# Kernel optimization log

Measured on AMD Instinct MI355X. Metric: run time of the kernel, lower is better.

Reference implementation:

```python
import jax, jax.numpy as jnp
import numpy as np

E = 256   # embed_dim
L = 64    # num_landmarks
C = 256   # in_channels
N_ITER = 6


def iterative_inv(K):
    # Newton-Schulz pseudo-inverse on small [*, L, L] matrices (faithful to torch code)
    I = jnp.eye(K.shape[-1], dtype=K.dtype)
    KA = jnp.abs(K)
    V0 = KA.sum(axis=-2, keepdims=True).max(axis=-1, keepdims=True)  # [*,1,1]
    VI = KA.sum(axis=-1, keepdims=True).max(axis=-2, keepdims=True)  # [*,1,1]
    V = jnp.swapaxes(K, -1, -2) / (V0 * VI)
    for _ in range(N_ITER):
        KV = K @ V
        V = 0.25 * V @ (13.0 * I - KV @ (15.0 * I - KV @ (7.0 * I - KV)))
    return V


def setup_inputs() -> dict:
    key = jax.random.key(0)
    k0, k1, k2 = jax.random.split(key, 3)
    x = jax.random.normal(k0, (8, C, 64, 64), dtype=jnp.float32)
    # Conv2d 1x1 weights stored as [out, in]
    w_qkv = jax.random.normal(k1, (3 * E, C), dtype=jnp.float32) * 0.02
    b_qkv = jnp.zeros((3 * E,), dtype=jnp.float32)
    w_out = jax.random.normal(k2, (C, E), dtype=jnp.float32) * 0.02
    b_out = jnp.zeros((C,), dtype=jnp.float32)
    return {"x": x, "w_qkv": w_qkv, "b_qkv": b_qkv, "w_out": w_out, "b_out": b_out}


def reference(x, w_qkv, b_qkv, w_out, b_out):
    N, Cin, H, W = x.shape
    HW = H * W
    # 1x1 conv: [N, 3E, H, W]
    y = jnp.einsum('nchw,ec->nehw', x, w_qkv) + b_qkv[None, :, None, None]
    # faithful raw reshape (mixes channel/spatial like the torch code)
    qkv = y.reshape(N, HW, 3 * E)
    q, k, v = jnp.split(qkv, 3, axis=-1)                     # each [N, HW, E]
    scale = HW ** 0.5
    q_land = q.reshape(N, L, HW // L, E).mean(axis=-2) / scale  # [N, L, E]
    k_land = k.reshape(N, L, HW // L, E).mean(axis=-2) / scale  # [N, L, E]
    # three softmaxes, all over dim=-2 as in the original
    k1 = jax.nn.softmax(jnp.einsum('nie,nje->nij', q, k_land), axis=-2)       # [N, HW, L]
    k2 = jax.nn.softmax(jnp.einsum('nie,nje->nij', q_land, k_land), axis=-2)  # [N, L, L]
    k3 = jax.nn.softmax(jnp.einsum('nie,nje->nij', q_land, k), axis=-2)       # [N, L, HW]
    k2_inv = iterative_inv(k2)
    out = k1 @ (k2_inv @ (k3 @ v)) + v                        # [N, HW, E]
    out = out.reshape(N, E, H, W)                             # faithful raw reshape
    return jnp.einsum('nehw,ce->nchw', out, w_out) + b_out[None, :, None, None]
```

## Files before the change

### kernel.cpp

```cpp
#include <hip/hip_runtime.h>
#include <hip/hip_bf16.h>

typedef unsigned short u16;
typedef __attribute__((ext_vector_type(4))) float f32x4;
typedef __attribute__((ext_vector_type(8))) short short8;

#define NB   8
#define CIN  256
#define EDIM 256
#define M3   768
#define HWN  4096
#define LND  64
#define NS2  72

__device__ __forceinline__ float bf2f(u16 u){ return __uint_as_float(((unsigned)u)<<16); }
__device__ __forceinline__ u16 f2bf(float f){ __hip_bfloat16 h = __float2bfloat16(f); return *reinterpret_cast<u16*>(&h); }
__device__ __forceinline__ void bf2x2(unsigned u, float &lo, float &hi){
  lo = __uint_as_float(u<<16);
  hi = __uint_as_float(u & 0xffff0000u);
}

typedef __attribute__((address_space(1))) unsigned as1_uint;
typedef __attribute__((address_space(3))) unsigned as3_uint;
__device__ __forceinline__ void gl16(const void* g, void* l){
  __builtin_amdgcn_global_load_lds((const as1_uint*)g, (as3_uint*)l, 16, 0, 0);
}

__global__ __launch_bounds__(256) void k_prep(const float* __restrict__ x, u16* __restrict__ Xt,
                                              const float* __restrict__ wq, const float* __restrict__ wo,
                                              u16* __restrict__ Wqb, u16* __restrict__ Wob){
  const int bi = blockIdx.x;
  const int tid = threadIdx.x;
  if(bi >= 2048){
    int ti = (bi-2048)*256 + tid;
    const float* src; u16* dst;
    if(ti < 1536){ src = wq + (size_t)ti*128;        dst = Wqb + (size_t)ti*128; }
    else         { src = wo + (size_t)(ti-1536)*128; dst = Wob + (size_t)(ti-1536)*128; }
    #pragma unroll
    for(int t=0;t<128;t+=8){
      float4 v0 = *(const float4*)(src+t);
      float4 v1 = *(const float4*)(src+t+4);
      ushort4 o0, o1;
      o0.x=f2bf(v0.x); o0.y=f2bf(v0.y); o0.z=f2bf(v0.z); o0.w=f2bf(v0.w);
      o1.x=f2bf(v1.x); o1.y=f2bf(v1.y); o1.z=f2bf(v1.z); o1.w=f2bf(v1.w);
      *(ushort4*)(dst+t)   = o0;
      *(ushort4*)(dst+t+4) = o1;
    }
    return;
  }
  __shared__ float Ts[64*65];
  const int n = bi>>8, rem = bi&255, ct = rem>>6, pt = rem&63;
  const int c0 = ct*64, p0 = pt*64;
  {
    int cc = tid>>2, pj = (tid&3)*16;
    const float* xp = x + (size_t)n*CIN*HWN + (size_t)(c0+cc)*HWN + p0 + pj;
    #pragma unroll
    for(int j=0;j<16;j++) Ts[cc*65 + pj + j] = xp[j];
  }
  __syncthreads();
  {
    int pp = tid>>2, ej = (tid&3)*16;
    u16* op = Xt + ((size_t)n*HWN + p0 + pp)*CIN + c0 + ej;
    ushort4 o[4];
    #pragma unroll
    for(int j=0;j<16;j++) ((u16*)o)[j] = f2bf(Ts[(ej+j)*65 + pp]);
    *(ushort4*)(op+0)  = o[0];
    *(ushort4*)(op+4)  = o[1];
    *(ushort4*)(op+8)  = o[2];
    *(ushort4*)(op+12) = o[3];
  }
}

__global__ __launch_bounds__(256) void k_qkv(const u16* __restrict__ Wb, const u16* __restrict__ Xt,
                                             const float* __restrict__ bias, u16* __restrict__ Y){
  __shared__ __align__(16) u16 As[128*64];
  __shared__ __align__(16) u16 Bs[128*64];
  const int bi = blockIdx.x;
  const int n = bi&7, rem = bi>>3;
  const int ch0 = (rem%6)*128, p0 = (rem/6)*128;
  const int tid = threadIdx.x, lane = tid&63;
  const int c = tid&15, qq = (tid>>4)&3, w4 = tid>>6;
  const int wr0 = (w4&1)*64, wc0 = (w4>>1)*64;
  const u16* xb = Xt + ((size_t)n*HWN + p0)*CIN;
  const u16* wb = Wb + (size_t)ch0*CIN;
  f32x4 acc[4][4];
  #pragma unroll
  for(int mt=0;mt<4;mt++)
    #pragma unroll
    for(int nt=0;nt<4;nt++){ acc[mt][nt][0]=0.f; acc[mt][nt][1]=0.f; acc[mt][nt][2]=0.f; acc[mt][nt][3]=0.f; }
  const int srow  = w4*8 + (lane>>3);
  const int dslot = lane&7;
  const int sgo   = (dslot ^ (lane>>3))*8;
  const int rdswz = (c&7);
  for(int ph=0; ph<4; ph++){
    #pragma unroll
    for(int j=0;j<4;j++){
      int r = j*32 + srow;
      gl16(wb + (size_t)r*CIN + ph*64 + sgo, &As[r*64 + dslot*8]);
    }
    #pragma unroll
    for(int j=0;j<4;j++){
      int r = j*32 + srow;
      gl16(xb + (size_t)r*CIN + ph*64 + sgo, &Bs[r*64 + dslot*8]);
    }
    __syncthreads();
    #pragma unroll
    for(int kt=0;kt<2;kt++){
      short8 af[4], bff[4];
      const int rslot = ((kt*4+qq)^rdswz)*8;
      #pragma unroll
      for(int mt=0;mt<4;mt++) af[mt]  = *(const short8*)&As[(wr0+mt*16+c)*64 + rslot];
      #pragma unroll
      for(int nt=0;nt<4;nt++) bff[nt] = *(const short8*)&Bs[(wc0+nt*16+c)*64 + rslot];
      #pragma unroll
      for(int mt=0;mt<4;mt++)
        #pragma unroll
        for(int nt=0;nt<4;nt++)
          acc[mt][nt] = __builtin_amdgcn_mfma_f32_16x16x32_bf16(af[mt], bff[nt], acc[mt][nt], 0, 0, 0);
    }
    __syncthreads();
  }
  u16* Yb = Y + (size_t)n*M3*HWN;
  #pragma unroll
  for(int mt=0;mt<4;mt++){
    int chb = ch0 + wr0 + mt*16 + 4*qq;
    float b0 = bias[chb], b1 = bias[chb+1], b2 = bias[chb+2], b3 = bias[chb+3];
    #pragma unroll
    for(int nt=0;nt<4;nt++){
      int p = p0 + wc0 + nt*16 + c;
      u16* yp = Yb + (size_t)chb*HWN + p;
      yp[0]             = f2bf(acc[mt][nt][0]+b0);
      yp[HWN]           = f2bf(acc[mt][nt][1]+b1);
      yp[2*(size_t)HWN] = f2bf(acc[mt][nt][2]+b2);
      yp[3*(size_t)HWN] = f2bf(acc[mt][nt][3]+b3);
    }
  }
}

__global__ void k_land(const u16* __restrict__ Y, float* __restrict__ qland, float* __restrict__ kland){
  const int l = blockIdx.x, n = blockIdx.y, e = threadIdx.x;
  const u16* base = Y + (size_t)n*M3*HWN;
  float qs=0.f, ks=0.f;
  #pragma unroll 8
  for(int m=0;m<64;m++){
    size_t off = (size_t)(l*64+m)*M3;
    qs += bf2f(base[off+e]);
    ks += bf2f(base[off+256+e]);
  }
  qland[((size_t)n*LND+l)*EDIM+e] = qs*(1.f/4096.f);
  kland[((size_t)n*LND+l)*EDIM+e] = ks*(1.f/4096.f);
}

__device__ __forceinline__ void ns_mm2(const u16* L, int sL, const u16* Rt, int sR,
                                       int wv, int q, int c, f32x4 r4[4]){
  short8 a0 = *(const short8*)(L + (size_t)(16*wv + c)*sL + 8*q);
  short8 a1 = *(const short8*)(L + (size_t)(16*wv + c)*sL + 32 + 8*q);
  #pragma unroll
  for(int tc=0;tc<4;tc++){
    f32x4 acc = {0.f,0.f,0.f,0.f};
    short8 b0 = *(const short8*)(Rt + (size_t)(16*tc + c)*sR + 8*q);
    short8 b1 = *(const short8*)(Rt + (size_t)(16*tc + c)*sR + 32 + 8*q);
    acc = __builtin_amdgcn_mfma_f32_16x16x32_bf16(a0, b0, acc, 0, 0, 0);
    acc = __builtin_amdgcn_mfma_f32_16x16x32_bf16(a1, b1, acc, 0, 0, 0);
    r4[tc] = acc;
  }
}

#define TTS 64
__device__ void ns_body(int n, char* smem, const float* __restrict__ qland,
                        const float* __restrict__ kland, float* __restrict__ KinvT){
  u16* Kb  = (u16*)(smem + 0);
  u16* Vb  = (u16*)(smem + 9216);
  u16* Vt  = (u16*)(smem + 18432);
  u16* KVb = (u16*)(smem + 27648);
  u16* KVt = (u16*)(smem + 36864);
  u16* Tt  = (u16*)(smem + 46080);
  float* sS   = (float*)(smem + 27648);
  float* sred = (float*)(smem + 44544);
  const int tid = threadIdx.x;
  const int wv = tid>>6, q = (tid>>4)&3, c = tid&15;
  const float* qb = qland + (size_t)n*LND*EDIM;
  const float* kb = kland + (size_t)n*LND*EDIM;
  f32x4 acc[4];
  #pragma unroll
  for(int t=0;t<4;t++){ acc[t][0]=0.f; acc[t][1]=0.f; acc[t][2]=0.f; acc[t][3]=0.f; }
  for(int e0=0;e0<EDIM;e0+=64){
    __syncthreads();
    {
      int row = tid>>2, c0 = (tid&3)*16;
      const float* qp = qb + (size_t)row*EDIM + e0 + c0;
      const float* kp = kb + (size_t)row*EDIM + e0 + c0;
      u16* qd = &KVb[row*NS2 + c0];
      u16* kd = &KVt[row*NS2 + c0];
      #pragma unroll
      for(int j=0;j<16;j+=4){
        float4 qv = *(const float4*)(qp+j);
        float4 kv = *(const float4*)(kp+j);
        ushort4 qo, ko;
        qo.x=f2bf(qv.x); qo.y=f2bf(qv.y); qo.z=f2bf(qv.z); qo.w=f2bf(qv.w);
        ko.x=f2bf(kv.x); ko.y=f2bf(kv.y); ko.z=f2bf(kv.z); ko.w=f2bf(kv.w);
        *(ushort4*)(qd+j) = qo;
        *(ushort4*)(kd+j) = ko;
      }
    }
    __syncthreads();
    {
      short8 a0 = *(const short8*)&KVb[(16*wv+c)*NS2 + 8*q];
      short8 a1 = *(const short8*)&KVb[(16*wv+c)*NS2 + 32 + 8*q];
      #pragma unroll
      for(int tc=0;tc<4;tc++){
        short8 b0 = *(const short8*)&KVt[(16*tc+c)*NS2 + 8*q];
        short8 b1 = *(const short8*)&KVt[(16*tc+c)*NS2 + 32 + 8*q];
        acc[tc] = __builtin_amdgcn_mfma_f32_16x16x32_bf16(a0, b0, acc[tc], 0, 0, 0);
        acc[tc] = __builtin_amdgcn_mfma_f32_16x16x32_bf16(a1, b1, acc[tc], 0, 0, 0);
      }
    }
  }
  __syncthreads();
  #pragma unroll
  for(int tc=0;tc<4;tc++){
    int col = 16*tc + c, row0 = 16*wv + 4*q;
    sS[(row0+0)*66+col] = acc[tc][0];
    sS[(row0+1)*66+col] = acc[tc][1];
    sS[(row0+2)*66+col] = acc[tc][2];
    sS[(row0+3)*66+col] = acc[tc][3];
  }
  __syncthreads();
  if(tid < 64){
    int j = tid;
    float m = -1e30f;
    for(int i=0;i<64;i++) m = fmaxf(m, sS[i*66+j]);
    float ssum = 0.f;
    for(int i=0;i<64;i++) ssum += __expf(sS[i*66+j]-m);
    float inv = 1.f/ssum, cs = 0.f;
    for(int i=0;i<64;i++){
      float kv = __expf(sS[i*66+j]-m)*inv;
      cs += fabsf(kv);
      Kb[i*NS2+j] = f2bf(kv);
    }
    sred[j] = cs;
  }
  __syncthreads();
  if(tid < 64){
    int i = tid; float rs = 0.f;
    for(int j=0;j<64;j++) rs += fabsf(bf2f(Kb[i*NS2+j]));
    sred[64+i] = rs;
  }
  __syncthreads();
  if(tid == 0){
    float v0=-1e30f, vi=-1e30f;
    for(int t=0;t<64;t++){ v0 = fmaxf(v0, sred[t]); vi = fmaxf(vi, sred[64+t]); }
    sred[128] = 1.f/(v0*vi);
  }
  __syncthreads();
  {
    float sc = sred[128];
    int i = tid>>2, j16 = (tid&3)*16;
    #pragma unroll
    for(int jj=0;jj<16;jj++){
      int j = j16+jj;
      u16 bvv = f2bf(bf2f(Kb[j*NS2+i])*sc);
      Vb[i*NS2+j] = bvv;
      Vt[j*NS2+i] = bvv;
    }
  }
  __syncthreads();
  f32x4 r4[4];
  for(int it=0; it<6; it++){
    ns_mm2(Kb, NS2, Vt, NS2, wv, q, c, r4);
    #pragma unroll
    for(int tc=0;tc<4;tc++){
      int col = 16*tc + c, row0 = 16*wv + 4*q;
      ushort4 pk;
      pk.x = f2bf(r4[tc][0]); pk.y = f2bf(r4[tc][1]); pk.z = f2bf(r4[tc][2]); pk.w = f2bf(r4[tc][3]);
      KVb[(row0+0)*NS2+col] = pk.x; KVb[(row0+1)*NS2+col] = pk.y;
      KVb[(row0+2)*NS2+col] = pk.z; KVb[(row0+3)*NS2+col] = pk.w;
      *(ushort4*)&KVt[(size_t)col*NS2 + row0] = pk;
    }
    __syncthreads();
    ns_mm2(KVb, NS2, KVt, NS2, wv, q, c, r4);
    #pragma unroll
    for(int tc=0;tc<4;tc++){
      int col = 16*tc+c, row0 = 16*wv+4*q;
      ushort4 pk;
      #pragma unroll
      for(int r=0;r<4;r++){
        float kvv = bf2f(KVb[(row0+r)*NS2+col]);
        ((u16*)&pk)[r] = f2bf(7.f*kvv - r4[tc][r]);
      }
      *(ushort4*)&Tt[(size_t)col*TTS + row0] = pk;
    }
    __syncthreads();
    ns_mm2(KVb, NS2, Tt, TTS, wv, q, c, r4);
    __syncthreads();
    #pragma unroll
    for(int tc=0;tc<4;tc++){
      int col = 16*tc+c, row0 = 16*wv+4*q;
      ushort4 pk;
      #pragma unroll
      for(int r=0;r<4;r++){
        float kvv = bf2f(KVb[(row0+r)*NS2+col]);
        ((u16*)&pk)[r] = f2bf(15.f*kvv - r4[tc][r]);
      }
      *(ushort4*)&Tt[(size_t)col*TTS + row0] = pk;
    }
    __syncthreads();
    ns_mm2(Vb, NS2, Tt, TTS, wv, q, c, r4);
    __syncthreads();
    #pragma unroll
    for(int tc=0;tc<4;tc++){
      int col = 16*tc+c, row0 = 16*wv+4*q;
      float nv[4]; ushort4 pk;
      #pragma unroll
      for(int r=0;r<4;r++){
        float vv = bf2f(Vb[(row0+r)*NS2+col]);
        nv[r] = 0.25f*(13.f*vv - r4[tc][r]);
        u16 bb = f2bf(nv[r]);
        Vb[(row0+r)*NS2+col] = bb;
        ((u16*)&pk)[r] = bb;
      }
      *(ushort4*)&Vt[(size_t)col*NS2 + row0] = pk;
      if(it==5){
        *(float4*)&KinvT[(size_t)n*4096 + (size_t)col*64 + row0] = make_float4(nv[0],nv[1],nv[2],nv[3]);
      }
    }
    __syncthreads();
  }
}

#define LGS 264
__global__ __launch_bounds__(256) void k_landgemm(const u16* __restrict__ Y, const float* __restrict__ qland,
                                                  const float* __restrict__ kland, float* __restrict__ Z1,
                                                  float* __restrict__ Z3, float* __restrict__ KinvT){
  __shared__ __align__(16) char usm[54272];
  const int z = blockIdx.y;
  if(blockIdx.x == 64){
    if((z&1)==0) ns_body(z>>1, usm, qland, kland, KinvT);
    return;
  }
  u16* As = (u16*)usm;
  u16* BsU = (u16*)(usm + 33792);
  const int n = z>>1, which = z&1;
  const int b0 = blockIdx.x*64;
  const float* land = (which ? qland : kland) + (size_t)n*LND*EDIM;
  const int boff = which ? 256 : 0;
  float* out = (which ? Z3 : Z1) + (size_t)n*LND*HWN;
  const u16* Yb = Y + (size_t)n*M3*HWN + boff;
  const int tid = threadIdx.x, lane = tid&63;
  const int c = tid&15, qq = (tid>>4)&3, wv = tid>>6;
  {
    int r = tid>>2, c0 = (tid&3)*64;
    const float* lp = land + (size_t)r*EDIM + c0;
    u16* dp = &As[r*LGS + c0];
    #pragma unroll
    for(int j=0;j<64;j+=4){
      float4 v = *(const float4*)(lp+j);
      ushort4 o; o.x=f2bf(v.x); o.y=f2bf(v.y); o.z=f2bf(v.z); o.w=f2bf(v.w);
      *(ushort4*)(dp+j) = o;
    }
  }
  const int srow  = wv*8 + (lane>>3);
  const int dslot = lane&7;
  const int sgo   = (dslot ^ (lane>>3))*8;
  const int rdswz = (c&7);
  f32x4 acc[4];
  #pragma unroll
  for(int nt=0;nt<4;nt++){ acc[nt][0]=0.f; acc[nt][1]=0.f; acc[nt][2]=0.f; acc[nt][3]=0.f; }
  #pragma unroll
  for(int j=0;j<2;j++){
    int r = j*32 + srow;
    gl16(Yb + (size_t)(b0+r)*M3 + sgo, BsU + r*64 + dslot*8);
  }
  __syncthreads();
  for(int ph=0; ph<4; ph++){
    const int cur = ph&1;
    if(ph<3){
      #pragma unroll
      for(int j=0;j<2;j++){
        int r = j*32 + srow;
        gl16(Yb + (size_t)(b0+r)*M3 + (ph+1)*64 + sgo, BsU + (cur^1)*4096 + r*64 + dslot*8);
      }
    }
    #pragma unroll
    for(int kt=0;kt<2;kt++){
      short8 af = *(const short8*)&As[(16*wv + c)*LGS + ph*64 + kt*32 + qq*8];
      const int rslot = ((kt*4+qq)^rdswz)*8;
      #pragma unroll
      for(int nt=0;nt<4;nt++){
        short8 bff = *(const short8*)&BsU[cur*4096 + (nt*16+c)*64 + rslot];
        acc[nt] = __builtin_amdgcn_mfma_f32_16x16x32_bf16(af, bff, acc[nt], 0, 0, 0);
      }
    }
    __syncthreads();
  }
  const int m0 = 16*wv + 4*qq;
  #pragma unroll
  for(int nt=0;nt<4;nt++){
    int col = b0 + nt*16 + c;
    out[(size_t)(m0+0)*HWN + col] = acc[nt][0];
    out[(size_t)(m0+1)*HWN + col] = acc[nt][1];
    out[(size_t)(m0+2)*HWN + col] = acc[nt][2];
    out[(size_t)(m0+3)*HWN + col] = acc[nt][3];
  }
}

__device__ void soft3_body(int idx, char* smem, const float* __restrict__ Z3, u16* __restrict__ P){
  const int kc = idx&31, n = idx>>5;
  const int tid = threadIdx.x, jb = kc*128;
  float* Sf   = (float*)smem;
  float* sinv = (float*)(smem + 33792);
  const float* z3b = Z3 + (size_t)n*LND*HWN;
  {
    int ibase = (tid>>5)*8, j4 = (tid&31)*4;
    #pragma unroll
    for(int r=0;r<8;r++){
      int i = ibase + r;
      *(float4*)&Sf[i*132 + j4] = *(const float4*)&z3b[(size_t)i*HWN + jb + j4];
    }
  }
  __syncthreads();
  if(tid < 128){
    int j = tid;
    float m = -1e30f;
    for(int i=0;i<64;i++) m = fmaxf(m, Sf[i*132 + j]);
    float s = 0.f;
    for(int i=0;i<64;i++){ float e = __expf(Sf[i*132 + j] - m); Sf[i*132 + j] = e; s += e; }
    sinv[j] = 1.f/s;
  }
  __syncthreads();
  {
    int i = tid>>2, j0 = (tid&3)*32;
    u16* pp = P + ((size_t)n*LND + i)*HWN + jb + j0;
    #pragma unroll
    for(int t=0;t<32;t+=4){
      ushort4 o;
      o.x = f2bf(Sf[i*132 + j0+t+0]*sinv[j0+t+0]);
      o.y = f2bf(Sf[i*132 + j0+t+1]*sinv[j0+t+1]);
      o.z = f2bf(Sf[i*132 + j0+t+2]*sinv[j0+t+2]);
      o.w = f2bf(Sf[i*132 + j0+t+3]*sinv[j0+t+3]);
      *(ushort4*)(pp+t) = o;
    }
  }
}

__device__ void soft1_body(int b, char* smem, float* __restrict__ Z1){
  const int n = b>>6, j = b&63, tid = threadIdx.x;
  float* redm = (float*)smem;
  float* reds = redm + 4;
  float* base = Z1 + ((size_t)n*LND + j)*HWN;
  float v[16];
  float m = -1e30f;
  #pragma unroll
  for(int r=0;r<16;r++){ v[r] = base[r*256 + tid]; m = fmaxf(m, v[r]); }
  #pragma unroll
  for(int o=32;o;o>>=1) m = fmaxf(m, __shfl_xor(m, o));
  const int wid = tid>>6;
  if((tid&63)==0) redm[wid] = m;
  __syncthreads();
  m = fmaxf(fmaxf(redm[0],redm[1]), fmaxf(redm[2],redm[3]));
  float s = 0.f;
  #pragma unroll
  for(int r=0;r<16;r++){ v[r] = __expf(v[r]-m); s += v[r]; }
  #pragma unroll
  for(int o=32;o;o>>=1) s += __shfl_xor(s, o);
  if((tid&63)==0) reds[wid] = s;
  __syncthreads();
  s = reds[0]+reds[1]+reds[2]+reds[3];
  float inv = 1.f/s;
  #pragma unroll
  for(int r=0;r<16;r++) base[r*256 + tid] = v[r]*inv;
}

__global__ __launch_bounds__(256) void k_mega(const float* __restrict__ Z3, u16* __restrict__ P,
                                              float* __restrict__ Z1){
  __shared__ __align__(16) char smem[34304];
  const int bi = blockIdx.x;
  if(bi < 256) soft3_body(bi, smem, Z3, P);
  else         soft1_body(bi-256, smem, Z1);
}

__global__ __launch_bounds__(256) void k_pv(const u16* __restrict__ P, const u16* __restrict__ Y,
                                            float* __restrict__ part){
  __shared__ __align__(16) u16 As[64*64];
  __shared__ __align__(16) u16 Vt[128*64];
  const int bi = blockIdx.x;
  const int kc = bi&31, n = (bi>>5)&7, eh = bi>>8;
  const int jb = kc*128, eb = eh*128;
  const int tid = threadIdx.x, lane = tid&63;
  const int c = tid&15, qq = (tid>>4)&3, wv = tid>>6;
  const u16* Pb = P + (size_t)n*LND*HWN;
  const u16* Yb = Y + (size_t)n*M3*HWN;
  const int srow  = wv*8 + (lane>>3);
  const int dslot = lane&7;
  const int sgo   = (dslot ^ (lane>>3))*8;
  const int rdswz = (c&7);
  f32x4 acc[4][2];
  #pragma unroll
  for(int mt=0;mt<4;mt++)
    #pragma unroll
    for(int nt=0;nt<2;nt++){ acc[mt][nt][0]=0.f; acc[mt][nt][1]=0.f; acc[mt][nt][2]=0.f; acc[mt][nt][3]=0.f; }
  for(int ph=0; ph<2; ph++){
    #pragma unroll
    for(int j=0;j<2;j++){
      int r = j*32 + srow;
      gl16(Pb + (size_t)r*HWN + jb + ph*64 + sgo, &As[r*64 + dslot*8]);
    }
    #pragma unroll
    for(int rep=0; rep<4; rep++){
      int jl = (tid>>4) + 16*rep;
      int ec = (tid&15)*8;
      uint4 U = *(const uint4*)&Yb[(size_t)(jb+ph*64+jl)*M3 + 512 + eb + ec];
      const u16* uv = (const u16*)&U;
      #pragma unroll
      for(int k=0;k<8;k++){
        int e = ec+k;
        int slot = ((jl>>3) ^ (e&7) ^ ((e>>3)&7)) & 7;
        Vt[e*64 + slot*8 + (jl&7)] = uv[k];
      }
    }
    __syncthreads();
    #pragma unroll
    for(int kt=0;kt<2;kt++){
      const int rslotA = ((kt*4+qq)^rdswz)*8;
      short8 af[4];
      #pragma unroll
      for(int mt=0;mt<4;mt++) af[mt] = *(const short8*)&As[(mt*16+c)*64 + rslotA];
      #pragma unroll
      for(int nt=0;nt<2;nt++){
        int e = wv*32 + nt*16 + c;
        int slotB = ((kt*4+qq) ^ (e&7) ^ ((e>>3)&7)) & 7;
        short8 bf_ = *(const short8*)&Vt[e*64 + slotB*8];
        #pragma unroll
        for(int mt=0;mt<4;mt++)
          acc[mt][nt] = __builtin_amdgcn_mfma_f32_16x16x32_bf16(af[mt], bf_, acc[mt][nt], 0, 0, 0);
      }
    }
    __syncthreads();
  }
  float* pb = part + ((size_t)n*32 + kc)*LND*EDIM + eb;
  #pragma unroll
  for(int mt=0;mt<4;mt++){
    int row0 = mt*16 + 4*qq;
    #pragma unroll
    for(int nt=0;nt<2;nt++){
      int e = wv*32 + nt*16 + c;
      pb[(size_t)(row0+0)*EDIM + e] = acc[mt][nt][0];
      pb[(size_t)(row0+1)*EDIM + e] = acc[mt][nt][1];
      pb[(size_t)(row0+2)*EDIM + e] = acc[mt][nt][2];
      pb[(size_t)(row0+3)*EDIM + e] = acc[mt][nt][3];
    }
  }
}

__global__ void k_fred(const float* __restrict__ part, float* __restrict__ B3){
  const int idx = blockIdx.x*256 + threadIdx.x;
  const int n = idx >> 14, rem = idx & 16383;
  const float* p = part + (size_t)n*32*16384 + rem;
  float s = 0.f;
  #pragma unroll
  for(int kc=0;kc<32;kc++) s += p[(size_t)kc*16384];
  B3[idx] = s;
}

__global__ __launch_bounds__(256) void k_c2(const float* __restrict__ KinvT, const float* __restrict__ B3,
                                            float* __restrict__ C2){
  const int eb = blockIdx.x*64, n = blockIdx.y, tid = threadIdx.x;
  __shared__ float KT[64][68];
  __shared__ float Bs2[64][68];
  {
    int l = tid>>2, o16 = (tid&3)*16;
    const float* kp = KinvT + (size_t)n*4096 + l*64 + o16;
    const float* bp = B3 + ((size_t)n*LND + l)*EDIM + eb + o16;
    #pragma unroll
    for(int t=0;t<16;t+=4){
      *(float4*)&KT[l][o16+t]  = *(const float4*)(kp+t);
      *(float4*)&Bs2[l][o16+t] = *(const float4*)(bp+t);
    }
  }
  __syncthreads();
  const int j0 = (tid>>4)*4, u0 = (tid&15)*4;
  float acc[4][4] = {};
  #pragma unroll 8
  for(int l=0;l<64;l++){
    f32x4 a = *(f32x4*)&KT[l][j0];
    f32x4 b = *(f32x4*)&Bs2[l][u0];
    #pragma unroll
    for(int s=0;s<4;s++)
      #pragma unroll
      for(int u=0;u<4;u++) acc[s][u] += a[s]*b[u];
  }
  #pragma unroll
  for(int s=0;s<4;s++){
    float4 fv = make_float4(acc[s][0],acc[s][1],acc[s][2],acc[s][3]);
    *(float4*)&C2[((size_t)n*LND + j0+s)*EDIM + eb + u0] = fv;
  }
}

__global__ __launch_bounds__(256) void k_out(const float* __restrict__ Z1, const float* __restrict__ C2,
                                             const u16* __restrict__ Y, u16* __restrict__ OM){
  const int ib = blockIdx.x*64, n = blockIdx.y, tid = threadIdx.x;
  __shared__ float K1s[64][68];
  __shared__ u16 C2s[64*264];
  {
    int j = tid>>2, i16 = (tid&3)*16;
    const float* zp = Z1 + ((size_t)n*LND + j)*HWN + ib + i16;
    #pragma unroll
    for(int t=0;t<16;t+=4) *(float4*)&K1s[j][i16+t] = *(const float4*)(zp+t);
    int e64 = (tid&3)*64;
    const float* cp = C2 + ((size_t)n*LND + j)*EDIM + e64;
    #pragma unroll
    for(int t=0;t<64;t+=4){
      float4 v = *(const float4*)(cp+t);
      C2s[j*264 + e64+t+0] = f2bf(v.x);
      C2s[j*264 + e64+t+1] = f2bf(v.y);
      C2s[j*264 + e64+t+2] = f2bf(v.z);
      C2s[j*264 + e64+t+3] = f2bf(v.w);
    }
  }
  __syncthreads();
  const int i0 = (tid>>4)*4, e0 = (tid&15)*16;
  float acc[4][16] = {};
  for(int j=0;j<64;j++){
    f32x4 a = *(f32x4*)&K1s[j][i0];
    const u16* cb = &C2s[j*264 + e0];
    uint4 U0 = *(const uint4*)cb;
    uint4 U1 = *(const uint4*)(cb+8);
    float bv[16];
    bf2x2(U0.x, bv[0], bv[1]);  bf2x2(U0.y, bv[2], bv[3]);
    bf2x2(U0.z, bv[4], bv[5]);  bf2x2(U0.w, bv[6], bv[7]);
    bf2x2(U1.x, bv[8], bv[9]);  bf2x2(U1.y, bv[10], bv[11]);
    bf2x2(U1.z, bv[12], bv[13]); bf2x2(U1.w, bv[14], bv[15]);
    #pragma unroll
    for(int u=0;u<16;u++){
      acc[0][u] += a[0]*bv[u];
      acc[1][u] += a[1]*bv[u];
      acc[2][u] += a[2]*bv[u];
      acc[3][u] += a[3]*bv[u];
    }
  }
  const u16* Yb = Y + (size_t)n*M3*HWN;
  u16* ob = OM + (size_t)n*HWN*EDIM;
  #pragma unroll
  for(int s=0;s<4;s++){
    int i = ib + i0 + s;
    const u16* vp = Yb + (size_t)i*M3 + 512 + e0;
    uint4 U0 = *(const uint4*)vp, U1 = *(const uint4*)(vp+8);
    float vv[16];
    bf2x2(U0.x, vv[0], vv[1]);  bf2x2(U0.y, vv[2], vv[3]);
    bf2x2(U0.z, vv[4], vv[5]);  bf2x2(U0.w, vv[6], vv[7]);
    bf2x2(U1.x, vv[8], vv[9]);  bf2x2(U1.y, vv[10], vv[11]);
    bf2x2(U1.z, vv[12], vv[13]); bf2x2(U1.w, vv[14], vv[15]);
    #pragma unroll
    for(int t=0;t<16;t+=4){
      ushort4 o;
      o.x = f2bf(acc[s][t+0]+vv[t+0]);
      o.y = f2bf(acc[s][t+1]+vv[t+1]);
      o.z = f2bf(acc[s][t+2]+vv[t+2]);
      o.w = f2bf(acc[s][t+3]+vv[t+3]);
      *(ushort4*)&ob[(size_t)i*EDIM + e0 + t] = o;
    }
  }
}

__global__ __launch_bounds__(256) void k_trans2(const u16* __restrict__ OM, u16* __restrict__ OMT){
  __shared__ u16 Ts[64*65];
  const int bi = blockIdx.x;
  const int n = bi>>8, rem = bi&255, et = rem>>6, pt = rem&63;
  const int e0 = et*64, p0 = pt*64, tid = threadIdx.x;
  const u16* omb = OM + (size_t)n*HWN*EDIM;
  {
    int ee = tid>>2, pj = (tid&3)*16;
    const u16* ip = omb + (size_t)(e0+ee)*HWN + p0 + pj;
    ushort4 v0 = *(const ushort4*)(ip);
    ushort4 v1 = *(const ushort4*)(ip+4);
    ushort4 v2 = *(const ushort4*)(ip+8);
    ushort4 v3 = *(const ushort4*)(ip+12);
    u16* tp = &Ts[ee*65 + pj];
    tp[0]=v0.x; tp[1]=v0.y; tp[2]=v0.z; tp[3]=v0.w;
    tp[4]=v1.x; tp[5]=v1.y; tp[6]=v1.z; tp[7]=v1.w;
    tp[8]=v2.x; tp[9]=v2.y; tp[10]=v2.z; tp[11]=v2.w;
    tp[12]=v3.x; tp[13]=v3.y; tp[14]=v3.z; tp[15]=v3.w;
  }
  __syncthreads();
  {
    int pp = tid>>2, ej = (tid&3)*16;
    u16* op = OMT + ((size_t)n*HWN + p0 + pp)*EDIM + e0 + ej;
    ushort4 o[4];
    #pragma unroll
    for(int j=0;j<16;j++) ((u16*)o)[j] = Ts[(ej+j)*65 + pp];
    *(ushort4*)(op+0)  = o[0];
    *(ushort4*)(op+4)  = o[1];
    *(ushort4*)(op+8)  = o[2];
    *(ushort4*)(op+12) = o[3];
  }
}

__global__ __launch_bounds__(256) void k_proj(const u16* __restrict__ Wb, const u16* __restrict__ OMT,
                                              const float* __restrict__ bias, float* __restrict__ out){
  __shared__ __align__(16) u16 As[128*64];
  __shared__ __align__(16) u16 Bs[128*64];
  const int bi = blockIdx.x;
  const int n = bi&7, rem = bi>>3;
  const int ch0 = (rem&1)*128, p0 = (rem>>1)*128;
  const int tid = threadIdx.x, lane = tid&63;
  const int c = tid&15, qq = (tid>>4)&3, w4 = tid>>6;
  const int wr0 = (w4&1)*64, wc0 = (w4>>1)*64;
  const u16* xb = OMT + ((size_t)n*HWN + p0)*EDIM;
  const u16* wb = Wb + (size_t)ch0*EDIM;
  f32x4 acc[4][4];
  #pragma unroll
  for(int mt=0;mt<4;mt++)
    #pragma unroll
    for(int nt=0;nt<4;nt++){ acc[mt][nt][0]=0.f; acc[mt][nt][1]=0.f; acc[mt][nt][2]=0.f; acc[mt][nt][3]=0.f; }
  const int srow  = w4*8 + (lane>>3);
  const int dslot = lane&7;
  const int sgo   = (dslot ^ (lane>>3))*8;
  const int rdswz = (c&7);
  for(int ph=0; ph<4; ph++){
    #pragma unroll
    for(int j=0;j<4;j++){
      int r = j*32 + srow;
      gl16(wb + (size_t)r*EDIM + ph*64 + sgo, &As[r*64 + dslot*8]);
    }
    #pragma unroll
    for(int j=0;j<4;j++){
      int r = j*32 + srow;
      gl16(xb + (size_t)r*EDIM + ph*64 + sgo, &Bs[r*64 + dslot*8]);
    }
    __syncthreads();
    #pragma unroll
    for(int kt=0;kt<2;kt++){
      short8 af[4], bff[4];
      const int rslot = ((kt*4+qq)^rdswz)*8;
      #pragma unroll
      for(int mt=0;mt<4;mt++) af[mt]  = *(const short8*)&As[(wr0+mt*16+c)*64 + rslot];
      #pragma unroll
      for(int nt=0;nt<4;nt++) bff[nt] = *(const short8*)&Bs[(wc0+nt*16+c)*64 + rslot];
      #pragma unroll
      for(int mt=0;mt<4;mt++)
        #pragma unroll
        for(int nt=0;nt<4;nt++)
          acc[mt][nt] = __builtin_amdgcn_mfma_f32_16x16x32_bf16(af[mt], bff[nt], acc[mt][nt], 0, 0, 0);
    }
    __syncthreads();
  }
  float* ob = out + (size_t)n*EDIM*HWN;
  #pragma unroll
  for(int mt=0;mt<4;mt++){
    int chb = ch0 + wr0 + mt*16 + 4*qq;
    float b0 = bias[chb], b1 = bias[chb+1], b2 = bias[chb+2], b3 = bias[chb+3];
    #pragma unroll
    for(int nt=0;nt<4;nt++){
      int p = p0 + wc0 + nt*16 + c;
      float* yp = ob + (size_t)chb*HWN + p;
      yp[0]             = acc[mt][nt][0]+b0;
      yp[HWN]           = acc[mt][nt][1]+b1;
      yp[2*(size_t)HWN] = acc[mt][nt][2]+b2;
      yp[3*(size_t)HWN] = acc[mt][nt][3]+b3;
    }
  }
}

extern "C" void kernel_launch(void* const* d_in, const int* in_sizes, int n_in,
                              void* d_out, int out_size, void* d_ws, size_t ws_size,
                              hipStream_t stream){
  (void)out_size; (void)ws_size;
  const float* x     = (const float*)d_in[0];
  const float* w_qkv = (const float*)d_in[1];
  const float* b_qkv = (const float*)d_in[2];
  const float* w_out = (const float*)d_in[3];
  const float* b_out = (const float*)d_in[4];
  for(int i=0;i<n_in;i++){
    switch(in_sizes[i]){
      case 8388608: x     = (const float*)d_in[i]; break;
      case 196608:  w_qkv = (const float*)d_in[i]; break;
      case 768:     b_qkv = (const float*)d_in[i]; break;
      case 65536:   w_out = (const float*)d_in[i]; break;
      case 256:     b_out = (const float*)d_in[i]; break;
      default: break;
    }
  }
  float* out = (float*)d_out;
  char* ws = (char*)d_ws;

  u16*   Y     = (u16*)(ws + 0);
  float* qland = (float*)(ws + 50331648);
  float* kland = (float*)(ws + 50855936);
  float* Z1    = (float*)(ws + 51380224);
  float* Z3    = (float*)(ws + 59768832);
  float* KinvT = (float*)(ws + 68157440);
  u16*   Xt    = (u16*)(ws + 68288512);
  float* part  = (float*)(ws + 68288512);
  u16*   OMT   = (u16*)(ws + 68288512);
  float* B3    = (float*)(ws + 85065728);
  float* C2    = (float*)(ws + 85590016);
  u16*   OM    = (u16*)(ws + 86114304);
  u16*   Pbuf  = (u16*)(ws + 86114304);
  u16*   Wqb   = (u16*)(ws + 59768832);
  u16*   Wob   = (u16*)(ws + 102891520);

  k_prep    <<<dim3(2056),   256, 0, stream>>>(x, Xt, w_qkv, w_out, Wqb, Wob);
  k_qkv     <<<dim3(1536),   256, 0, stream>>>(Wqb, Xt, b_qkv, Y);
  k_land    <<<dim3(64,8),   256, 0, stream>>>(Y, qland, kland);
  k_landgemm<<<dim3(65,16),  256, 0, stream>>>(Y, qland, kland, Z1, Z3, KinvT);
  k_mega    <<<dim3(768),    256, 0, stream>>>(Z3, Pbuf, Z1);
  k_pv      <<<dim3(512),    256, 0, stream>>>(Pbuf, Y, part);
  k_fred    <<<dim3(512),    256, 0, stream>>>(part, B3);
  k_c2      <<<dim3(4,8),    256, 0, stream>>>(KinvT, B3, C2);
  k_out     <<<dim3(64,8),   256, 0, stream>>>(Z1, C2, Y, OM);
  k_trans2  <<<dim3(2048),   256, 0, stream>>>(OM, OMT);
  k_proj    <<<dim3(512),    256, 0, stream>>>(Wob, OMT, b_out, out);
}
```

Before: 220.8 us.

## Fuse split-K reduction into k_c2, use MFMA in k_out, drop transpose kernel

New measurement: 211.5 us. -4.2%, faster.

```diff
diff --git a/kernel.cpp b/kernel.cpp
--- a/kernel.cpp
+++ b/kernel.cpp
@@ -552,30 +552,34 @@
   }
 }
 
-__global__ void k_fred(const float* __restrict__ part, float* __restrict__ B3){
-  const int idx = blockIdx.x*256 + threadIdx.x;
-  const int n = idx >> 14, rem = idx & 16383;
-  const float* p = part + (size_t)n*32*16384 + rem;
-  float s = 0.f;
-  #pragma unroll
-  for(int kc=0;kc<32;kc++) s += p[(size_t)kc*16384];
-  B3[idx] = s;
-}
-
-__global__ __launch_bounds__(256) void k_c2(const float* __restrict__ KinvT, const float* __restrict__ B3,
-                                            float* __restrict__ C2){
+__global__ __launch_bounds__(256) void k_c2(const float* __restrict__ KinvT, const float* __restrict__ part,
+                                            u16* __restrict__ C2T){
   const int eb = blockIdx.x*64, n = blockIdx.y, tid = threadIdx.x;
   __shared__ float KT[64][68];
   __shared__ float Bs2[64][68];
+  __shared__ u16 Ct[64*72];
   {
     int l = tid>>2, o16 = (tid&3)*16;
     const float* kp = KinvT + (size_t)n*4096 + l*64 + o16;
-    const float* bp = B3 + ((size_t)n*LND + l)*EDIM + eb + o16;
-    #pragma unroll
-    for(int t=0;t<16;t+=4){
-      *(float4*)&KT[l][o16+t]  = *(const float4*)(kp+t);
-      *(float4*)&Bs2[l][o16+t] = *(const float4*)(bp+t);
-    }
+    #pragma unroll
+    for(int t=0;t<16;t+=4) *(float4*)&KT[l][o16+t] = *(const float4*)(kp+t);
+    const float* pp = part + (size_t)n*32*16384 + (size_t)l*256 + eb + o16;
+    float4 s0 = {0,0,0,0}, s1 = {0,0,0,0}, s2 = {0,0,0,0}, s3 = {0,0,0,0};
+    for(int kc=0;kc<32;kc++){
+      const float* b = pp + (size_t)kc*16384;
+      float4 v0 = *(const float4*)(b);
+      float4 v1 = *(const float4*)(b+4);
+      float4 v2 = *(const float4*)(b+8);
+      float4 v3 = *(const float4*)(b+12);
+      s0.x+=v0.x; s0.y+=v0.y; s0.z+=v0.z; s0.w+=v0.w;
+      s1.x+=v1.x; s1.y+=v1.y; s1.z+=v1.z; s1.w+=v1.w;
+      s2.x+=v2.x; s2.y+=v2.y; s2.z+=v2.z; s2.w+=v2.w;
+      s3.x+=v3.x; s3.y+=v3.y; s3.z+=v3.z; s3.w+=v3.w;
+    }
+    *(float4*)&Bs2[l][o16+0]  = s0;
+    *(float4*)&Bs2[l][o16+4]  = s1;
+    *(float4*)&Bs2[l][o16+8]  = s2;
+    *(float4*)&Bs2[l][o16+12] = s3;
   }
   __syncthreads();
   const int j0 = (tid>>4)*4, u0 = (tid&15)*4;
@@ -590,122 +594,99 @@
       for(int u=0;u<4;u++) acc[s][u] += a[s]*b[u];
   }
   #pragma unroll
-  for(int s=0;s<4;s++){
-    float4 fv = make_float4(acc[s][0],acc[s][1],acc[s][2],acc[s][3]);
-    *(float4*)&C2[((size_t)n*LND + j0+s)*EDIM + eb + u0] = fv;
-  }
-}
-
-__global__ __launch_bounds__(256) void k_out(const float* __restrict__ Z1, const float* __restrict__ C2,
+  for(int s=0;s<4;s++)
+    #pragma unroll
+    for(int u=0;u<4;u++)
+      Ct[(u0+u)*72 + j0+s] = f2bf(acc[s][u]);
+  __syncthreads();
+  {
+    int e = tid>>2, j16 = (tid&3)*16;
+    u16* op = C2T + ((size_t)n*256 + eb + e)*64 + j16;
+    #pragma unroll
+    for(int t=0;t<16;t+=4)
+      *(ushort4*)(op+t) = *(const ushort4*)&Ct[e*72 + j16 + t];
+  }
+}
+
+__global__ __launch_bounds__(256) void k_out(const float* __restrict__ Z1, const u16* __restrict__ C2T,
                                              const u16* __restrict__ Y, u16* __restrict__ OM){
-  const int ib = blockIdx.x*64, n = blockIdx.y, tid = threadIdx.x;
-  __shared__ float K1s[64][68];
-  __shared__ u16 C2s[64*264];
+  __shared__ __align__(16) u16 Cs[256*64];
+  __shared__ __align__(16) u16 Zt[64*72];
+  const int ib = blockIdx.x*64, n = blockIdx.y;
+  const int tid = threadIdx.x, lane = tid&63;
+  const int c = tid&15, qq = (tid>>4)&3, wv = tid>>6;
+  const int srow  = wv*8 + (lane>>3);
+  const int dslot = lane&7;
+  const int sgo   = (dslot ^ (lane>>3))*8;
+  const int rdswz = (c&7);
+  const u16* cb = C2T + (size_t)n*256*64;
+  #pragma unroll
+  for(int j=0;j<8;j++){
+    int r = j*32 + srow;
+    gl16(cb + (size_t)r*64 + sgo, &Cs[r*64 + dslot*8]);
+  }
   {
     int j = tid>>2, i16 = (tid&3)*16;
     const float* zp = Z1 + ((size_t)n*LND + j)*HWN + ib + i16;
     #pragma unroll
-    for(int t=0;t<16;t+=4) *(float4*)&K1s[j][i16+t] = *(const float4*)(zp+t);
-    int e64 = (tid&3)*64;
-    const float* cp = C2 + ((size_t)n*LND + j)*EDIM + e64;
-    #pragma unroll
-    for(int t=0;t<64;t+=4){
-      float4 v = *(const float4*)(cp+t);
-      C2s[j*264 + e64+t+0] = f2bf(v.x);
-      C2s[j*264 + e64+t+1] = f2bf(v.y);
-      C2s[j*264 + e64+t+2] = f2bf(v.z);
-      C2s[j*264 + e64+t+3] = f2bf(v.w);
-    }
-  }
-  __syncthreads();
-  const int i0 = (tid>>4)*4, e0 = (tid&15)*16;
-  float acc[4][16] = {};
-  for(int j=0;j<64;j++){
-    f32x4 a = *(f32x4*)&K1s[j][i0];
-    const u16* cb = &C2s[j*264 + e0];
-    uint4 U0 = *(const uint4*)cb;
-    uint4 U1 = *(const uint4*)(cb+8);
-    float bv[16];
-    bf2x2(U0.x, bv[0], bv[1]);  bf2x2(U0.y, bv[2], bv[3]);
-    bf2x2(U0.z, bv[4], bv[5]);  bf2x2(U0.w, bv[6], bv[7]);
-    bf2x2(U1.x, bv[8], bv[9]);  bf2x2(U1.y, bv[10], bv[11]);
-    bf2x2(U1.z, bv[12], bv[13]); bf2x2(U1.w, bv[14], bv[15]);
-    #pragma unroll
-    for(int u=0;u<16;u++){
-      acc[0][u] += a[0]*bv[u];
-      acc[1][u] += a[1]*bv[u];
-      acc[2][u] += a[2]*bv[u];
-      acc[3][u] += a[3]*bv[u];
-    }
+    for(int t=0;t<16;t+=4){
+      float4 v = *(const float4*)(zp+t);
+      Zt[(i16+t+0)*72 + j] = f2bf(v.x);
+      Zt[(i16+t+1)*72 + j] = f2bf(v.y);
+      Zt[(i16+t+2)*72 + j] = f2bf(v.z);
+      Zt[(i16+t+3)*72 + j] = f2bf(v.w);
+    }
+  }
+  __syncthreads();
+  f32x4 acc[4][4];
+  #pragma unroll
+  for(int mt=0;mt<4;mt++)
+    #pragma unroll
+    for(int nt=0;nt<4;nt++){ acc[mt][nt][0]=0.f; acc[mt][nt][1]=0.f; acc[mt][nt][2]=0.f; acc[mt][nt][3]=0.f; }
+  #pragma unroll
+  for(int kt=0;kt<2;kt++){
+    const int rslot = ((kt*4+qq)^rdswz)*8;
+    short8 af[4], bf_[4];
+    #pragma unroll
+    for(int mt=0;mt<4;mt++) af[mt] = *(const short8*)&Cs[(wv*64+mt*16+c)*64 + rslot];
+    #pragma unroll
+    for(int nt=0;nt<4;nt++) bf_[nt] = *(const short8*)&Zt[(nt*16+c)*72 + kt*32 + qq*8];
+    #pragma unroll
+    for(int mt=0;mt<4;mt++)
+      #pragma unroll
+      for(int nt=0;nt<4;nt++)
+        acc[mt][nt] = __builtin_amdgcn_mfma_f32_16x16x32_bf16(af[mt], bf_[nt], acc[mt][nt], 0, 0, 0);
   }
   const u16* Yb = Y + (size_t)n*M3*HWN;
   u16* ob = OM + (size_t)n*HWN*EDIM;
   #pragma unroll
-  for(int s=0;s<4;s++){
-    int i = ib + i0 + s;
-    const u16* vp = Yb + (size_t)i*M3 + 512 + e0;
-    uint4 U0 = *(const uint4*)vp, U1 = *(const uint4*)(vp+8);
-    float vv[16];
-    bf2x2(U0.x, vv[0], vv[1]);  bf2x2(U0.y, vv[2], vv[3]);
-    bf2x2(U0.z, vv[4], vv[5]);  bf2x2(U0.w, vv[6], vv[7]);
-    bf2x2(U1.x, vv[8], vv[9]);  bf2x2(U1.y, vv[10], vv[11]);
-    bf2x2(U1.z, vv[12], vv[13]); bf2x2(U1.w, vv[14], vv[15]);
-    #pragma unroll
-    for(int t=0;t<16;t+=4){
+  for(int mt=0;mt<4;mt++){
+    int e = wv*64 + mt*16 + 4*qq;
+    #pragma unroll
+    for(int nt=0;nt<4;nt++){
+      int i = ib + nt*16 + c;
+      ushort4 V4 = *(const ushort4*)(Yb + (size_t)i*M3 + 512 + e);
       ushort4 o;
-      o.x = f2bf(acc[s][t+0]+vv[t+0]);
-      o.y = f2bf(acc[s][t+1]+vv[t+1]);
-      o.z = f2bf(acc[s][t+2]+vv[t+2]);
-      o.w = f2bf(acc[s][t+3]+vv[t+3]);
-      *(ushort4*)&ob[(size_t)i*EDIM + e0 + t] = o;
-    }
-  }
-}
-
-__global__ __launch_bounds__(256) void k_trans2(const u16* __restrict__ OM, u16* __restrict__ OMT){
-  __shared__ u16 Ts[64*65];
-  const int bi = blockIdx.x;
-  const int n = bi>>8, rem = bi&255, et = rem>>6, pt = rem&63;
-  const int e0 = et*64, p0 = pt*64, tid = threadIdx.x;
-  const u16* omb = OM + (size_t)n*HWN*EDIM;
-  {
-    int ee = tid>>2, pj = (tid&3)*16;
-    const u16* ip = omb + (size_t)(e0+ee)*HWN + p0 + pj;
-    ushort4 v0 = *(const ushort4*)(ip);
-    ushort4 v1 = *(const ushort4*)(ip+4);
-    ushort4 v2 = *(const ushort4*)(ip+8);
-    ushort4 v3 = *(const ushort4*)(ip+12);
-    u16* tp = &Ts[ee*65 + pj];
-    tp[0]=v0.x; tp[1]=v0.y; tp[2]=v0.z; tp[3]=v0.w;
-    tp[4]=v1.x; tp[5]=v1.y; tp[6]=v1.z; tp[7]=v1.w;
-    tp[8]=v2.x; tp[9]=v2.y; tp[10]=v2.z; tp[11]=v2.w;
-    tp[12]=v3.x; tp[13]=v3.y; tp[14]=v3.z; tp[15]=v3.w;
-  }
-  __syncthreads();
-  {
-    int pp = tid>>2, ej = (tid&3)*16;
-    u16* op = OMT + ((size_t)n*HWN + p0 + pp)*EDIM + e0 + ej;
-    ushort4 o[4];
-    #pragma unroll
-    for(int j=0;j<16;j++) ((u16*)o)[j] = Ts[(ej+j)*65 + pp];
-    *(ushort4*)(op+0)  = o[0];
-    *(ushort4*)(op+4)  = o[1];
-    *(ushort4*)(op+8)  = o[2];
-    *(ushort4*)(op+12) = o[3];
-  }
-}
-
-__global__ __launch_bounds__(256) void k_proj(const u16* __restrict__ Wb, const u16* __restrict__ OMT,
+      o.x = f2bf(acc[mt][nt][0] + bf2f(V4.x));
+      o.y = f2bf(acc[mt][nt][1] + bf2f(V4.y));
+      o.z = f2bf(acc[mt][nt][2] + bf2f(V4.z));
+      o.w = f2bf(acc[mt][nt][3] + bf2f(V4.w));
+      *(ushort4*)(ob + (size_t)i*EDIM + e) = o;
+    }
+  }
+}
+
+__global__ __launch_bounds__(256) void k_proj(const u16* __restrict__ Wb, const u16* __restrict__ OM,
                                               const float* __restrict__ bias, float* __restrict__ out){
   __shared__ __align__(16) u16 As[128*64];
-  __shared__ __align__(16) u16 Bs[128*64];
+  __shared__ __align__(16) u16 Bt[128*64];
   const int bi = blockIdx.x;
   const int n = bi&7, rem = bi>>3;
   const int ch0 = (rem&1)*128, p0 = (rem>>1)*128;
   const int tid = threadIdx.x, lane = tid&63;
   const int c = tid&15, qq = (tid>>4)&3, w4 = tid>>6;
   const int wr0 = (w4&1)*64, wc0 = (w4>>1)*64;
-  const u16* xb = OMT + ((size_t)n*HWN + p0)*EDIM;
+  const u16* omb = OM + (size_t)n*HWN*EDIM;
   const u16* wb = Wb + (size_t)ch0*EDIM;
   f32x4 acc[4][4];
   #pragma unroll
@@ -723,19 +704,31 @@
       gl16(wb + (size_t)r*EDIM + ph*64 + sgo, &As[r*64 + dslot*8]);
     }
     #pragma unroll
-    for(int j=0;j<4;j++){
-      int r = j*32 + srow;
-      gl16(xb + (size_t)r*EDIM + ph*64 + sgo, &Bs[r*64 + dslot*8]);
+    for(int rep=0; rep<4; rep++){
+      int ee = (tid>>4) + 16*rep;
+      int pc = (tid&15)*8;
+      uint4 U = *(const uint4*)&omb[(size_t)(ph*64+ee)*HWN + p0 + pc];
+      const u16* uv = (const u16*)&U;
+      #pragma unroll
+      for(int k=0;k<8;k++){
+        int p = pc+k;
+        int slot = ((ee>>3) ^ (p&7) ^ ((p>>3)&7)) & 7;
+        Bt[p*64 + slot*8 + (ee&7)] = uv[k];
+      }
     }
     __syncthreads();
     #pragma unroll
     for(int kt=0;kt<2;kt++){
+      const int rslot = ((kt*4+qq)^rdswz)*8;
       short8 af[4], bff[4];
-      const int rslot = ((kt*4+qq)^rdswz)*8;
-      #pragma unroll
-      for(int mt=0;mt<4;mt++) af[mt]  = *(const short8*)&As[(wr0+mt*16+c)*64 + rslot];
-      #pragma unroll
-      for(int nt=0;nt<4;nt++) bff[nt] = *(const short8*)&Bs[(wc0+nt*16+c)*64 + rslot];
+      #pragma unroll
+      for(int mt=0;mt<4;mt++) af[mt] = *(const short8*)&As[(wr0+mt*16+c)*64 + rslot];
+      #pragma unroll
+      for(int nt=0;nt<4;nt++){
+        int p = wc0 + nt*16 + c;
+        int slotB = ((kt*4+qq) ^ (p&7) ^ ((p>>3)&7)) & 7;
+        bff[nt] = *(const short8*)&Bt[p*64 + slotB*8];
+      }
       #pragma unroll
       for(int mt=0;mt<4;mt++)
         #pragma unroll
@@ -789,11 +782,9 @@
   float* Z1    = (float*)(ws + 51380224);
   float* Z3    = (float*)(ws + 59768832);
   float* KinvT = (float*)(ws + 68157440);
+  float* part  = (float*)(ws + 68288512);
   u16*   Xt    = (u16*)(ws + 68288512);
-  float* part  = (float*)(ws + 68288512);
-  u16*   OMT   = (u16*)(ws + 68288512);
-  float* B3    = (float*)(ws + 85065728);
-  float* C2    = (float*)(ws + 85590016);
+  u16*   C2T   = (u16*)(ws + 85065728);
   u16*   OM    = (u16*)(ws + 86114304);
   u16*   Pbuf  = (u16*)(ws + 86114304);
   u16*   Wqb   = (u16*)(ws + 59768832);
@@ -805,9 +796,7 @@
   k_landgemm<<<dim3(65,16),  256, 0, stream>>>(Y, qland, kland, Z1, Z3, KinvT);
   k_mega    <<<dim3(768),    256, 0, stream>>>(Z3, Pbuf, Z1);
   k_pv      <<<dim3(512),    256, 0, stream>>>(Pbuf, Y, part);
-  k_fred    <<<dim3(512),    256, 0, stream>>>(part, B3);
-  k_c2      <<<dim3(4,8),    256, 0, stream>>>(KinvT, B3, C2);
-  k_out     <<<dim3(64,8),   256, 0, stream>>>(Z1, C2, Y, OM);
-  k_trans2  <<<dim3(2048),   256, 0, stream>>>(OM, OMT);
-  k_proj    <<<dim3(512),    256, 0, stream>>>(Wob, OMT, b_out, out);
-}
+  k_c2      <<<dim3(4,8),    256, 0, stream>>>(KinvT, part, C2T);
+  k_out     <<<dim3(64,8),   256, 0, stream>>>(Z1, C2T, Y, OM);
+  k_proj    <<<dim3(512),    256, 0, stream>>>(Wob, OM, b_out, out);
+}
```
